# Kernel optimization log

Hardware: AMD Instinct MI355X
Metric: run time of the kernel (lower is better)

Reference implementation:

```python
import jax, jax.numpy as jnp
import numpy as np

N_EMBD = 2048
HEAD_DIM = 128
N_CTX = 2048
BATCH = 8
SEQ = 2048


def setup_inputs() -> dict:
    key = jax.random.key(0)
    ks = jax.random.split(key, 7)
    s = 1.0 / np.sqrt(N_EMBD)
    x = jax.random.normal(ks[0], (BATCH, SEQ, N_EMBD), dtype=jnp.float32)
    # torch Linear params: weight (out, in), bias (out,)
    Wq = jax.random.uniform(ks[1], (HEAD_DIM, N_EMBD), jnp.float32, -s, s)
    bq = jax.random.uniform(ks[2], (HEAD_DIM,), jnp.float32, -s, s)
    Wk = jax.random.uniform(ks[3], (HEAD_DIM, N_EMBD), jnp.float32, -s, s)
    bk = jax.random.uniform(ks[4], (HEAD_DIM,), jnp.float32, -s, s)
    Wv = jax.random.uniform(ks[5], (HEAD_DIM, N_EMBD), jnp.float32, -s, s)
    bv = jax.random.uniform(ks[6], (HEAD_DIM,), jnp.float32, -s, s)
    return {"x": x, "Wq": Wq, "bq": bq, "Wk": Wk, "bk": bk, "Wv": Wv, "bv": bv}


def reference(x, Wq, bq, Wk, bk, Wv, bv):
    # projections: y = x @ W^T + b
    q = jnp.einsum('bse,de->bsd', x, Wq) + bq  # (B, S, D)
    k = jnp.einsum('bse,de->bsd', x, Wk) + bk
    v = jnp.einsum('bse,de->bsd', x, Wv) + bv
    seq = x.shape[1]
    scores = jnp.einsum('bqd,bkd->bqk', q, k)  # (B, S, S)
    # causal mask: strictly-upper-triangular positions set to -inf (before scaling, as in source)
    causal = jnp.triu(jnp.ones((seq, seq), dtype=bool), k=1)
    scores = jnp.where(causal[None, :, :], -jnp.inf, scores)
    # NOTE: source scales by sqrt(seq_size), not sqrt(head_dim)
    weight = jax.nn.softmax(scores / jnp.sqrt(jnp.float32(seq)), axis=-1)
    return jnp.einsum('bqk,bkd->bqd', weight, v)
```

## Files before the change

### kernel.cpp

```cpp
#include <hip/hip_runtime.h>
#include <cmath>

#define BATCH 8
#define SEQ   2048
#define NEMB  2048
#define HD    128
#define NROWS (BATCH * SEQ)

typedef __bf16 v8bf __attribute__((ext_vector_type(8)));
typedef float  f32x4 __attribute__((ext_vector_type(4)));

union U8 { v8bf v; __bf16 b[8]; unsigned short e[8]; };
union F4 { f32x4 v; float f[4]; };

__device__ inline void async16(void* lds, const void* g) {
  __builtin_amdgcn_global_load_lds(
      (const __attribute__((address_space(1))) unsigned int*)g,
      (__attribute__((address_space(3))) unsigned int*)lds, 16, 0, 0);
}

__device__ inline v8bf cvt8(float4 a, float4 b) {
  U8 u;
  u.b[0] = (__bf16)a.x; u.b[1] = (__bf16)a.y; u.b[2] = (__bf16)a.z; u.b[3] = (__bf16)a.w;
  u.b[4] = (__bf16)b.x; u.b[5] = (__bf16)b.y; u.b[6] = (__bf16)b.z; u.b[7] = (__bf16)b.w;
  return u.v;
}

__global__ __launch_bounds__(256) void wconv_kernel(
    const float* __restrict__ Wq, const float* __restrict__ Wk,
    const float* __restrict__ Wv, __bf16* __restrict__ out) {
  const int id = blockIdx.x;
  const int proj = id >> 6, blk = id & 63;
  const float* __restrict__ W = proj == 0 ? Wq : proj == 1 ? Wk : Wv;
  __bf16* __restrict__ o = out + (size_t)proj * (HD * NEMB);
  const int base = blk * 4096 + threadIdx.x * 16;
  const float4* s = (const float4*)(W + base);
  float4 f0 = s[0], f1 = s[1], f2 = s[2], f3 = s[3];
  *(v8bf*)(o + base) = cvt8(f0, f1);
  *(v8bf*)(o + base + 8) = cvt8(f2, f3);
}

__global__ __launch_bounds__(256, 3) void qkv_proj_kernel(
    const float* __restrict__ x, const __bf16* __restrict__ Wb,
    const float* __restrict__ bq, const float* __restrict__ bk,
    const float* __restrict__ bv,
    __bf16* __restrict__ Qb, __bf16* __restrict__ Kb, __bf16* __restrict__ Vb)
{
  const int bid0 = blockIdx.x;
  const int bid = ((bid0 & 7) * 48) + (bid0 >> 3);
  const int mt = bid / 3;
  const int proj = bid % 3;
  const __bf16* __restrict__ W = Wb + (size_t)proj * (HD * NEMB);
  const float* __restrict__ bias = proj == 0 ? bq : proj == 1 ? bk : bv;
  __bf16* __restrict__ Out = proj == 0 ? Qb : proj == 1 ? Kb : Vb;
  const int m0 = mt * 128;

  __shared__ float  Asm[128 * 64];
  __shared__ __bf16 Bsm[128 * 64];

  const int t = threadIdx.x, lane = t & 63, w = t >> 6;
  const int wm = w >> 1, wn = w & 1;
  const int hi = lane >> 4, lo = lane & 15;

  const float* pa[8];
  char* la[8];
#pragma unroll
  for (int i = 0; i < 8; ++i) {
    const int j = w * 8 + i;
    const int r = j * 4 + (lane >> 4);
    const int c = (lane & 15) ^ (r & 7);
    pa[i] = x + (size_t)(m0 + r) * NEMB + c * 4;
    la[i] = (char*)Asm + j * 1024;
  }
  const __bf16* pb[4];
  char* lb[4];
#pragma unroll
  for (int i = 0; i < 4; ++i) {
    const int j = w * 4 + i;
    const int r = j * 8 + (lane >> 3);
    const int c = (lane & 7) ^ (r & 7);
    pb[i] = W + (size_t)r * NEMB + c * 8;
    lb[i] = (char*)Bsm + j * 1024;
  }

  f32x4 acc[4][4];
  const f32x4 fz = {0.f, 0.f, 0.f, 0.f};
#pragma unroll
  for (int m = 0; m < 4; ++m)
#pragma unroll
    for (int n = 0; n < 4; ++n) acc[m][n] = fz;

  for (int tt = 0; tt < NEMB / 64; ++tt) {
    const int k0 = tt * 64;
    __syncthreads();
#pragma unroll
    for (int i = 0; i < 8; ++i) async16(la[i], pa[i] + k0);
#pragma unroll
    for (int i = 0; i < 4; ++i) async16(lb[i], pb[i] + k0);
    __syncthreads();

#pragma unroll
    for (int kk = 0; kk < 2; ++kk) {
      v8bf a[4], b[4];
#pragma unroll
      for (int m = 0; m < 4; ++m) {
        const int r = wm * 64 + m * 16 + lo;
        const int s = kk * 8 + hi * 2;
        const char* rowp = (const char*)Asm + r * 256;
        F4 a0, a1;
        a0.v = *(const f32x4*)(rowp + (((s)     ^ (r & 7)) << 4));
        a1.v = *(const f32x4*)(rowp + (((s + 1) ^ (r & 7)) << 4));
        U8 u;
#pragma unroll
        for (int q = 0; q < 4; ++q) {
          u.b[q]     = (__bf16)a0.f[q];
          u.b[q + 4] = (__bf16)a1.f[q];
        }
        a[m] = u.v;
      }
#pragma unroll
      for (int n = 0; n < 4; ++n) {
        const int r = wn * 64 + n * 16 + lo;
        const int kc = kk * 4 + hi;
        b[n] = *(const v8bf*)((const char*)Bsm + r * 128 + ((kc ^ (r & 7)) << 4));
      }
#pragma unroll
      for (int m = 0; m < 4; ++m)
#pragma unroll
        for (int n = 0; n < 4; ++n)
          acc[m][n] = __builtin_amdgcn_mfma_f32_16x16x32_bf16(a[m], b[n], acc[m][n], 0, 0, 0);
    }
  }

#pragma unroll
  for (int n = 0; n < 4; ++n) {
    const int col = wn * 64 + n * 16 + lo;
    const float bi = bias[col];
#pragma unroll
    for (int m = 0; m < 4; ++m) {
#pragma unroll
      for (int r = 0; r < 4; ++r) {
        const int row = m0 + wm * 64 + m * 16 + hi * 4 + r;
        Out[(size_t)row * HD + col] = (__bf16)(acc[m][n][r] + bi);
      }
    }
  }
}

__global__ __launch_bounds__(256) void attn_kernel(
    const __bf16* __restrict__ Qb, const __bf16* __restrict__ Kb,
    const __bf16* __restrict__ Vb, __bf16* __restrict__ Opart,
    float* __restrict__ Ml)
{
  const int bid0 = blockIdx.x;
  const int bid = ((bid0 & 7) << 7) + (bid0 >> 3);
  const int b = bid >> 7;
  const int q = bid & 127;
  const int qt = q >> 2;
  const int s  = q & 3;
  const int q0 = qt * 64;
  const int kv_beg = (s * (qt + 1)) >> 2;
  const int kv_end = ((s + 1) * (qt + 1)) >> 2;
  const int nst = kv_end - kv_beg;

  const int t = threadIdx.x, lane = t & 63, w = t >> 6;
  const int hi = lane >> 4, lo = lane & 15;

  __shared__ __bf16 Ksm[2][64 * 128];
  __shared__ __bf16 Vtsm[2][128 * 64];
  __shared__ __bf16 Psm[4][16 * 64];

  v8bf aQ[4];
  {
    const __bf16* qp = Qb + ((size_t)(b * SEQ + q0 + w * 16 + lo)) * HD + hi * 8;
#pragma unroll
    for (int kk = 0; kk < 4; ++kk) aQ[kk] = *(const v8bf*)(qp + kk * 32);
  }

  const __bf16* kga[4];
#pragma unroll
  for (int i = 0; i < 4; ++i) {
    const int r = (w * 4 + i) * 4 + (lane >> 4);
    const int c = (lane & 15) ^ (r & 7);
    kga[i] = Kb + ((size_t)(b * SEQ) + r) * HD + c * 8;
  }

  const int keyg = t >> 4, dg = t & 15;
  U8 vv[4];

  f32x4 accO[8];
  const f32x4 fz = {0.f, 0.f, 0.f, 0.f};
#pragma unroll
  for (int n = 0; n < 8; ++n) accO[n] = fz;
  float m_s[4], l_s[4];
#pragma unroll
  for (int r = 0; r < 4; ++r) { m_s[r] = -INFINITY; l_s[r] = 0.f; }

  const float scale = 0.022097086912079608f;

  if (nst > 0) {
    auto STAGE_K = [&](int kv, int buf) {
      const size_t off = (size_t)kv * 64 * HD;
      char* kb = (char*)&Ksm[buf][0];
#pragma unroll
      for (int i = 0; i < 4; ++i) async16(kb + (w * 4 + i) * 1024, kga[i] + off);
    };
    auto LOAD_V = [&](int kv) {
      const __bf16* vp = Vb + ((size_t)(b * SEQ + kv * 64 + keyg * 4)) * HD + dg * 8;
#pragma unroll
      for (int j = 0; j < 4; ++j) vv[j].v = *(const v8bf*)(vp + (size_t)j * HD);
    };
    auto WRITE_VT = [&](int buf) {
      char* vb2 = (char*)&Vtsm[buf][0];
#pragma unroll
      for (int dd = 0; dd < 8; ++dd) {
        const int d = (dd + dg) & 7;
        ushort4 pk = make_ushort4(vv[0].e[d], vv[1].e[d], vv[2].e[d], vv[3].e[d]);
        const int row = dg * 8 + d;
        *(ushort4*)(vb2 + row * 128 + ((keyg * 8) ^ ((row & 7) << 4))) = pk;
      }
    };

    STAGE_K(kv_beg, 0);
    LOAD_V(kv_beg);
    WRITE_VT(0);
    __syncthreads();

    for (int t2 = 0; t2 < nst; ++t2) {
      const int kv = kv_beg + t2;
      const int cur = t2 & 1;
      const bool more = (t2 + 1 < nst);
      if (more) { STAGE_K(kv + 1, cur ^ 1); LOAD_V(kv + 1); }

      f32x4 accS[4];
#pragma unroll
      for (int n = 0; n < 4; ++n) accS[n] = fz;
      const char* ksm = (const char*)&Ksm[cur][0];
#pragma unroll
      for (int kk = 0; kk < 4; ++kk) {
        const int cb = kk * 64 + hi * 16;
        v8bf bk[4];
#pragma unroll
        for (int n = 0; n < 4; ++n) {
          const int r = n * 16 + lo;
          bk[n] = *(const v8bf*)(ksm + r * 256 + (cb ^ ((r & 7) << 4)));
        }
#pragma unroll
        for (int n = 0; n < 4; ++n)
          accS[n] = __builtin_amdgcn_mfma_f32_16x16x32_bf16(aQ[kk], bk[n], accS[n], 0, 0, 0);
      }

      float sv[4][4];
      const bool diag = (kv == qt);
#pragma unroll
      for (int n = 0; n < 4; ++n)
#pragma unroll
        for (int r = 0; r < 4; ++r) {
          float v = accS[n][r] * scale;
          if (diag) {
            const int key = kv * 64 + n * 16 + lo;
            const int qr = q0 + w * 16 + hi * 4 + r;
            if (key > qr) v = -INFINITY;
          }
          sv[n][r] = v;
        }

      float mx[4];
#pragma unroll
      for (int r = 0; r < 4; ++r) {
        mx[r] = fmaxf(fmaxf(sv[0][r], sv[1][r]), fmaxf(sv[2][r], sv[3][r]));
#pragma unroll
        for (int off = 1; off < 16; off <<= 1)
          mx[r] = fmaxf(mx[r], __shfl_xor(mx[r], off));
      }
      float corr[4], p[4][4], rs[4];
#pragma unroll
      for (int r = 0; r < 4; ++r) {
        const float mnew = fmaxf(m_s[r], mx[r]);
        corr[r] = __expf(m_s[r] - mnew);
        m_s[r] = mnew;
        rs[r] = 0.f;
      }
#pragma unroll
      for (int n = 0; n < 4; ++n)
#pragma unroll
        for (int r = 0; r < 4; ++r) {
          p[n][r] = __expf(sv[n][r] - m_s[r]);
          rs[r] += p[n][r];
        }
#pragma unroll
      for (int r = 0; r < 4; ++r) {
#pragma unroll
        for (int off = 1; off < 16; off <<= 1) rs[r] += __shfl_xor(rs[r], off);
        l_s[r] = l_s[r] * corr[r] + rs[r];
      }
#pragma unroll
      for (int n = 0; n < 8; ++n)
#pragma unroll
        for (int r = 0; r < 4; ++r) accO[n][r] *= corr[r];

#pragma unroll
      for (int n = 0; n < 4; ++n)
#pragma unroll
        for (int r = 0; r < 4; ++r) {
          const int row = hi * 4 + r;
          __bf16 h = (__bf16)p[n][r];
          *(unsigned short*)((char*)&Psm[w][0] + row * 128 +
                             (((n * 16 + lo) * 2) ^ ((row & 7) << 4))) =
              __builtin_bit_cast(unsigned short, h);
        }

      if (more) WRITE_VT(cur ^ 1);

      const char* vsm = (const char*)&Vtsm[cur][0];
#pragma unroll
      for (int k2 = 0; k2 < 2; ++k2) {
        const int cb = k2 * 64 + hi * 16;
        const v8bf aP = *(const v8bf*)((const char*)&Psm[w][0] + lo * 128 + (cb ^ ((lo & 7) << 4)));
#pragma unroll
        for (int n = 0; n < 8; ++n) {
          const int r = n * 16 + lo;
          const v8bf bv = *(const v8bf*)(vsm + r * 128 + (cb ^ ((r & 7) << 4)));
          accO[n] = __builtin_amdgcn_mfma_f32_16x16x32_bf16(aP, bv, accO[n], 0, 0, 0);
        }
      }
      if (more) __syncthreads();
    }
  }

#pragma unroll
  for (int r = 0; r < 4; ++r) {
    const int qr = q0 + w * 16 + hi * 4 + r;
    __bf16* op = Opart + ((size_t)s * NROWS + b * SEQ + qr) * HD + lo;
#pragma unroll
    for (int n = 0; n < 8; ++n) op[n * 16] = (__bf16)accO[n][r];
    if (lo == 0) {
      float* mlp = Ml + ((size_t)s * NROWS + b * SEQ + qr) * 2;
      mlp[0] = m_s[r];
      mlp[1] = l_s[r];
    }
  }
}

__global__ __launch_bounds__(256) void combine_kernel(
    const __bf16* __restrict__ Opart, const float* __restrict__ Ml,
    float* __restrict__ out)
{
  const int idx = blockIdx.x * 256 + threadIdx.x;
  const int row = idx >> 2, ch = idx & 3;
  float m[4], l[4];
#pragma unroll
  for (int s = 0; s < 4; ++s) {
    const float* mlp = Ml + ((size_t)s * NROWS + row) * 2;
    m[s] = mlp[0];
    l[s] = mlp[1];
  }
  const float M = fmaxf(fmaxf(m[0], m[1]), fmaxf(m[2], m[3]));
  float e[4], denom = 0.f;
#pragma unroll
  for (int s = 0; s < 4; ++s) { e[s] = __expf(m[s] - M); denom += l[s] * e[s]; }
  const float inv = 1.f / denom;

  float* po = out + (size_t)row * HD + ch * 32;
#pragma unroll
  for (int j = 0; j < 4; ++j) {
    float sum[8];
#pragma unroll
    for (int q2 = 0; q2 < 8; ++q2) sum[q2] = 0.f;
#pragma unroll
    for (int s = 0; s < 4; ++s) {
      U8 o;
      o.v = *(const v8bf*)(Opart + ((size_t)s * NROWS + row) * HD + ch * 32 + j * 8);
#pragma unroll
      for (int q2 = 0; q2 < 8; ++q2) sum[q2] += (float)o.b[q2] * e[s];
    }
#pragma unroll
    for (int q2 = 0; q2 < 8; ++q2) po[j * 8 + q2] = sum[q2] * inv;
  }
}

extern "C" void kernel_launch(void* const* d_in, const int* in_sizes, int n_in,
                              void* d_out, int out_size, void* d_ws, size_t ws_size,
                              hipStream_t stream) {
  const float* x  = (const float*)d_in[0];
  const float* Wq = (const float*)d_in[1];
  const float* bq = (const float*)d_in[2];
  const float* Wk = (const float*)d_in[3];
  const float* bk = (const float*)d_in[4];
  const float* Wv = (const float*)d_in[5];
  const float* bv = (const float*)d_in[6];
  float* out = (float*)d_out;

  __bf16* Qb = (__bf16*)d_ws;
  __bf16* Kb = Qb + (size_t)NROWS * HD;
  __bf16* Vb = Kb + (size_t)NROWS * HD;
  __bf16* Wb = Vb + (size_t)NROWS * HD;
  __bf16* Opart = Wb + (size_t)3 * HD * NEMB;
  float*  Ml = (float*)(Opart + (size_t)4 * NROWS * HD);

  wconv_kernel<<<dim3(3 * 64), dim3(256), 0, stream>>>(Wq, Wk, Wv, Wb);
  qkv_proj_kernel<<<dim3(128 * 3), dim3(256), 0, stream>>>(
      x, Wb, bq, bk, bv, Qb, Kb, Vb);
  attn_kernel<<<dim3(BATCH * 32 * 4), dim3(256), 0, stream>>>(Qb, Kb, Vb, Opart, Ml);
  combine_kernel<<<dim3(NROWS * 4 / 256), dim3(256), 0, stream>>>(Opart, Ml, out);
}
```

Measured before the change: 116.8 us.

## Triple-buffer QKV projection LDS tiles with async prefetch two stages ahead

Converts the QKV projection GEMM main loop from a single-buffered load-sync-compute pattern to a three-stage LDS ring buffer. Tiles for k-step tt+2 are issued via async global-to-LDS loads while step tt computes, with vmcnt waits gating consumption. The aim is to hide global memory latency behind MFMA work. The cost is 144KB of LDS per block, which forces occupancy down to one block per CU, so latency hiding relies entirely on the pipeline.

After: 136.0 us. +16.5%, slower.

```diff
diff --git a/kernel.cpp b/kernel.cpp
--- a/kernel.cpp
+++ b/kernel.cpp
@@ -40,7 +40,7 @@
   *(v8bf*)(o + base + 8) = cvt8(f2, f3);
 }
 
-__global__ __launch_bounds__(256, 3) void qkv_proj_kernel(
+__global__ __launch_bounds__(256, 1) void qkv_proj_kernel(
     const float* __restrict__ x, const __bf16* __restrict__ Wb,
     const float* __restrict__ bq, const float* __restrict__ bk,
     const float* __restrict__ bv,
@@ -55,32 +55,31 @@
   __bf16* __restrict__ Out = proj == 0 ? Qb : proj == 1 ? Kb : Vb;
   const int m0 = mt * 128;
 
-  __shared__ float  Asm[128 * 64];
-  __shared__ __bf16 Bsm[128 * 64];
+  __shared__ char smem[147456];
 
   const int t = threadIdx.x, lane = t & 63, w = t >> 6;
   const int wm = w >> 1, wn = w & 1;
   const int hi = lane >> 4, lo = lane & 15;
 
   const float* pa[8];
-  char* la[8];
+  int laOff[8];
 #pragma unroll
   for (int i = 0; i < 8; ++i) {
     const int j = w * 8 + i;
     const int r = j * 4 + (lane >> 4);
     const int c = (lane & 15) ^ (r & 7);
     pa[i] = x + (size_t)(m0 + r) * NEMB + c * 4;
-    la[i] = (char*)Asm + j * 1024;
+    laOff[i] = j * 1024;
   }
   const __bf16* pb[4];
-  char* lb[4];
+  int lbOff[4];
 #pragma unroll
   for (int i = 0; i < 4; ++i) {
     const int j = w * 4 + i;
     const int r = j * 8 + (lane >> 3);
     const int c = (lane & 7) ^ (r & 7);
     pb[i] = W + (size_t)r * NEMB + c * 8;
-    lb[i] = (char*)Bsm + j * 1024;
+    lbOff[i] = 32768 + j * 1024;
   }
 
   f32x4 acc[4][4];
@@ -90,15 +89,17 @@
 #pragma unroll
     for (int n = 0; n < 4; ++n) acc[m][n] = fz;
 
-  for (int tt = 0; tt < NEMB / 64; ++tt) {
+  auto STAGE = [&](int tt, int buf) {
     const int k0 = tt * 64;
-    __syncthreads();
-#pragma unroll
-    for (int i = 0; i < 8; ++i) async16(la[i], pa[i] + k0);
-#pragma unroll
-    for (int i = 0; i < 4; ++i) async16(lb[i], pb[i] + k0);
-    __syncthreads();
-
+    char* base = smem + buf * 49152;
+#pragma unroll
+    for (int i = 0; i < 8; ++i) async16(base + laOff[i], pa[i] + k0);
+#pragma unroll
+    for (int i = 0; i < 4; ++i) async16(base + lbOff[i], pb[i] + k0);
+  };
+  auto COMPUTE = [&](int buf) {
+    const char* Ab = smem + buf * 49152;
+    const char* Bb = Ab + 32768;
 #pragma unroll
     for (int kk = 0; kk < 2; ++kk) {
       v8bf a[4], b[4];
@@ -106,7 +107,7 @@
       for (int m = 0; m < 4; ++m) {
         const int r = wm * 64 + m * 16 + lo;
         const int s = kk * 8 + hi * 2;
-        const char* rowp = (const char*)Asm + r * 256;
+        const char* rowp = Ab + r * 256;
         F4 a0, a1;
         a0.v = *(const f32x4*)(rowp + (((s)     ^ (r & 7)) << 4));
         a1.v = *(const f32x4*)(rowp + (((s + 1) ^ (r & 7)) << 4));
@@ -122,7 +123,7 @@
       for (int n = 0; n < 4; ++n) {
         const int r = wn * 64 + n * 16 + lo;
         const int kc = kk * 4 + hi;
-        b[n] = *(const v8bf*)((const char*)Bsm + r * 128 + ((kc ^ (r & 7)) << 4));
+        b[n] = *(const v8bf*)(Bb + r * 128 + ((kc ^ (r & 7)) << 4));
       }
 #pragma unroll
       for (int m = 0; m < 4; ++m)
@@ -130,6 +131,22 @@
         for (int n = 0; n < 4; ++n)
           acc[m][n] = __builtin_amdgcn_mfma_f32_16x16x32_bf16(a[m], b[n], acc[m][n], 0, 0, 0);
     }
+  };
+
+  const int NT = NEMB / 64;
+  STAGE(0, 0);
+  STAGE(1, 1);
+  for (int tt = 0; tt < NT; ++tt) {
+    if (tt < NT - 1) {
+      asm volatile("s_waitcnt vmcnt(12)" ::: "memory");
+    } else {
+      asm volatile("s_waitcnt vmcnt(0)" ::: "memory");
+    }
+    __builtin_amdgcn_sched_barrier(0);
+    __builtin_amdgcn_s_barrier();
+    COMPUTE(tt % 3);
+    __builtin_amdgcn_s_barrier();
+    if (tt + 2 < NT) STAGE(tt + 2, (tt + 2) % 3);
   }
 
 #pragma unroll
```

## Split-K the QKV projection with smaller M tiles and a bias-adding reduce kernel

Applied to the files above, without the earlier changes.

The projection GEMM now halves the row tile to 64 and splits the 2048-wide reduction into two halves, raising the grid from 384 to 1536 blocks and the occupancy hint from 3 to 5. The goal is to fill the CUs better than 1.5 waves of large blocks did. Each half writes a bf16 partial result to a new workspace area. A separate reduce kernel then sums the two partials and adds the bias to produce Q, K and V. The cost is an extra launch, extra global traffic for the partials, and an additional bf16 rounding step before the sum.

Measured after the change: 121.2 us. 3.8% more time.

```diff
diff --git a/kernel.cpp b/kernel.cpp
--- a/kernel.cpp
+++ b/kernel.cpp
@@ -40,71 +40,69 @@
   *(v8bf*)(o + base + 8) = cvt8(f2, f3);
 }
 
-__global__ __launch_bounds__(256, 3) void qkv_proj_kernel(
+__global__ __launch_bounds__(256, 5) void qkv_proj_kernel(
     const float* __restrict__ x, const __bf16* __restrict__ Wb,
-    const float* __restrict__ bq, const float* __restrict__ bk,
-    const float* __restrict__ bv,
-    __bf16* __restrict__ Qb, __bf16* __restrict__ Kb, __bf16* __restrict__ Vb)
+    __bf16* __restrict__ Opp)
 {
   const int bid0 = blockIdx.x;
-  const int bid = ((bid0 & 7) * 48) + (bid0 >> 3);
-  const int mt = bid / 3;
-  const int proj = bid % 3;
+  const int bid = ((bid0 & 7) * 192) + (bid0 >> 3);
+  const int mt = bid / 6;
+  const int rem = bid % 6;
+  const int proj = rem >> 1;
+  const int kh = rem & 1;
   const __bf16* __restrict__ W = Wb + (size_t)proj * (HD * NEMB);
-  const float* __restrict__ bias = proj == 0 ? bq : proj == 1 ? bk : bv;
-  __bf16* __restrict__ Out = proj == 0 ? Qb : proj == 1 ? Kb : Vb;
-  const int m0 = mt * 128;
-
-  __shared__ float  Asm[128 * 64];
+  const int m0 = mt * 64;
+  const int kbase = kh * 1024;
+
+  __shared__ float  Asm[64 * 64];
   __shared__ __bf16 Bsm[128 * 64];
 
   const int t = threadIdx.x, lane = t & 63, w = t >> 6;
   const int wm = w >> 1, wn = w & 1;
   const int hi = lane >> 4, lo = lane & 15;
 
-  const float* pa[8];
-  char* la[8];
-#pragma unroll
-  for (int i = 0; i < 8; ++i) {
-    const int j = w * 8 + i;
-    const int r = j * 4 + (lane >> 4);
-    const int c = (lane & 15) ^ (r & 7);
-    pa[i] = x + (size_t)(m0 + r) * NEMB + c * 4;
-    la[i] = (char*)Asm + j * 1024;
-  }
+  const float* pa[4];
   const __bf16* pb[4];
+  char* la[4];
   char* lb[4];
 #pragma unroll
   for (int i = 0; i < 4; ++i) {
-    const int j = w * 4 + i;
-    const int r = j * 8 + (lane >> 3);
-    const int c = (lane & 7) ^ (r & 7);
-    pb[i] = W + (size_t)r * NEMB + c * 8;
-    lb[i] = (char*)Bsm + j * 1024;
-  }
-
-  f32x4 acc[4][4];
+    {
+      const int r = (w * 4 + i) * 4 + (lane >> 4);
+      const int c = (lane & 15) ^ (r & 7);
+      pa[i] = x + (size_t)(m0 + r) * NEMB + kbase + c * 4;
+      la[i] = (char*)Asm + (w * 4 + i) * 1024;
+    }
+    {
+      const int r = (w * 4 + i) * 8 + (lane >> 3);
+      const int c = (lane & 7) ^ (r & 7);
+      pb[i] = W + (size_t)r * NEMB + kbase + c * 8;
+      lb[i] = (char*)Bsm + (w * 4 + i) * 1024;
+    }
+  }
+
+  f32x4 acc[2][4];
   const f32x4 fz = {0.f, 0.f, 0.f, 0.f};
 #pragma unroll
-  for (int m = 0; m < 4; ++m)
+  for (int m = 0; m < 2; ++m)
 #pragma unroll
     for (int n = 0; n < 4; ++n) acc[m][n] = fz;
 
-  for (int tt = 0; tt < NEMB / 64; ++tt) {
+  for (int tt = 0; tt < 16; ++tt) {
     const int k0 = tt * 64;
     __syncthreads();
 #pragma unroll
-    for (int i = 0; i < 8; ++i) async16(la[i], pa[i] + k0);
+    for (int i = 0; i < 4; ++i) async16(la[i], pa[i] + k0);
 #pragma unroll
     for (int i = 0; i < 4; ++i) async16(lb[i], pb[i] + k0);
     __syncthreads();
 
 #pragma unroll
     for (int kk = 0; kk < 2; ++kk) {
-      v8bf a[4], b[4];
-#pragma unroll
-      for (int m = 0; m < 4; ++m) {
-        const int r = wm * 64 + m * 16 + lo;
+      v8bf a[2], b[4];
+#pragma unroll
+      for (int m = 0; m < 2; ++m) {
+        const int r = wm * 32 + m * 16 + lo;
         const int s = kk * 8 + hi * 2;
         const char* rowp = (const char*)Asm + r * 256;
         F4 a0, a1;
@@ -125,26 +123,46 @@
         b[n] = *(const v8bf*)((const char*)Bsm + r * 128 + ((kc ^ (r & 7)) << 4));
       }
 #pragma unroll
-      for (int m = 0; m < 4; ++m)
+      for (int m = 0; m < 2; ++m)
 #pragma unroll
         for (int n = 0; n < 4; ++n)
           acc[m][n] = __builtin_amdgcn_mfma_f32_16x16x32_bf16(a[m], b[n], acc[m][n], 0, 0, 0);
     }
   }
 
+  __bf16* op = Opp + ((size_t)(kh * 3 + proj) * NROWS + m0) * HD;
 #pragma unroll
   for (int n = 0; n < 4; ++n) {
     const int col = wn * 64 + n * 16 + lo;
-    const float bi = bias[col];
-#pragma unroll
-    for (int m = 0; m < 4; ++m) {
+#pragma unroll
+    for (int m = 0; m < 2; ++m) {
 #pragma unroll
       for (int r = 0; r < 4; ++r) {
-        const int row = m0 + wm * 64 + m * 16 + hi * 4 + r;
-        Out[(size_t)row * HD + col] = (__bf16)(acc[m][n][r] + bi);
-      }
-    }
-  }
+        const int row = wm * 32 + m * 16 + hi * 4 + r;
+        op[(size_t)row * HD + col] = (__bf16)acc[m][n][r];
+      }
+    }
+  }
+}
+
+__global__ __launch_bounds__(256) void reduce_kernel(
+    const __bf16* __restrict__ Opp, const float* __restrict__ bq,
+    const float* __restrict__ bk, const float* __restrict__ bv,
+    __bf16* __restrict__ QKV)
+{
+  const size_t g = (size_t)blockIdx.x * 256 + threadIdx.x;
+  const size_t f = g * 8;
+  const int proj = (int)(f / ((size_t)NROWS * HD));
+  const int col = (int)(f & (HD - 1));
+  const float* __restrict__ bias = proj == 0 ? bq : proj == 1 ? bk : bv;
+  U8 p0, p1;
+  p0.v = *(const v8bf*)(Opp + f);
+  p1.v = *(const v8bf*)(Opp + (size_t)3 * NROWS * HD + f);
+  U8 o;
+#pragma unroll
+  for (int j = 0; j < 8; ++j)
+    o.b[j] = (__bf16)((float)p0.b[j] + (float)p1.b[j] + bias[col + j]);
+  *(v8bf*)(QKV + f) = o.v;
 }
 
 __global__ __launch_bounds__(256) void attn_kernel(
@@ -395,12 +413,14 @@
   __bf16* Kb = Qb + (size_t)NROWS * HD;
   __bf16* Vb = Kb + (size_t)NROWS * HD;
   __bf16* Wb = Vb + (size_t)NROWS * HD;
-  __bf16* Opart = Wb + (size_t)3 * HD * NEMB;
+  __bf16* Opp = Wb + (size_t)3 * HD * NEMB;
+  __bf16* Opart = Opp + (size_t)6 * NROWS * HD;
   float*  Ml = (float*)(Opart + (size_t)4 * NROWS * HD);
 
   wconv_kernel<<<dim3(3 * 64), dim3(256), 0, stream>>>(Wq, Wk, Wv, Wb);
-  qkv_proj_kernel<<<dim3(128 * 3), dim3(256), 0, stream>>>(
-      x, Wb, bq, bk, bv, Qb, Kb, Vb);
+  qkv_proj_kernel<<<dim3(1536), dim3(256), 0, stream>>>(x, Wb, Opp);
+  reduce_kernel<<<dim3(3 * NROWS * HD / (256 * 8)), dim3(256), 0, stream>>>(
+      Opp, bq, bk, bv, Qb);
   attn_kernel<<<dim3(BATCH * 32 * 4), dim3(256), 0, stream>>>(Qb, Kb, Vb, Opart, Ml);
   combine_kernel<<<dim3(NROWS * 4 / 256), dim3(256), 0, stream>>>(Opart, Ml, out);
 }
```

## Fuse QKV projections per tile with split-K and fp16 partial reduction

Applied to the files above, without the earlier changes.

The projection kernel now computes Q, K and V together in one 128x384 tile per block, so each x tile is loaded once instead of three times. K is split in half across blocks, giving 256 blocks of 512 threads. Each block writes fp16 partial sums, and a new reduce kernel adds the two halves plus the bias and writes the bf16 Q/K/V. This trades repeated fp32 x traffic for an extra kernel launch, partial-sum memory traffic and a larger workspace, with some risk to fp16 range and precision.

Result: slower. 127.0 us (+8.7%).

```diff
diff --git a/kernel.cpp b/kernel.cpp
--- a/kernel.cpp
+++ b/kernel.cpp
@@ -9,6 +9,7 @@
 
 typedef __bf16 v8bf __attribute__((ext_vector_type(8)));
 typedef float  f32x4 __attribute__((ext_vector_type(4)));
+typedef _Float16 v8h __attribute__((ext_vector_type(8)));
 
 union U8 { v8bf v; __bf16 b[8]; unsigned short e[8]; };
 union F4 { f32x4 v; float f[4]; };
@@ -40,73 +41,71 @@
   *(v8bf*)(o + base + 8) = cvt8(f2, f3);
 }
 
-__global__ __launch_bounds__(256, 3) void qkv_proj_kernel(
+__global__ __launch_bounds__(512, 2) void qkv_proj_kernel(
     const float* __restrict__ x, const __bf16* __restrict__ Wb,
-    const float* __restrict__ bq, const float* __restrict__ bk,
-    const float* __restrict__ bv,
-    __bf16* __restrict__ Qb, __bf16* __restrict__ Kb, __bf16* __restrict__ Vb)
+    _Float16* __restrict__ Opp)
 {
   const int bid0 = blockIdx.x;
-  const int bid = ((bid0 & 7) * 48) + (bid0 >> 3);
-  const int mt = bid / 3;
-  const int proj = bid % 3;
-  const __bf16* __restrict__ W = Wb + (size_t)proj * (HD * NEMB);
-  const float* __restrict__ bias = proj == 0 ? bq : proj == 1 ? bk : bv;
-  __bf16* __restrict__ Out = proj == 0 ? Qb : proj == 1 ? Kb : Vb;
+  const int bid = ((bid0 & 7) << 5) + (bid0 >> 3);
+  const int mt = bid >> 1;
+  const int kh = bid & 1;
   const int m0 = mt * 128;
-
-  __shared__ float  Asm[128 * 64];
-  __shared__ __bf16 Bsm[128 * 64];
+  const int kbase = kh * 1024;
+
+  __shared__ char smem[81920];
+  char* const Asm = smem;
+  char* const Bsm = smem + 32768;
 
   const int t = threadIdx.x, lane = t & 63, w = t >> 6;
-  const int wm = w >> 1, wn = w & 1;
+  const int wm = w >> 2, wn4 = w & 3;
   const int hi = lane >> 4, lo = lane & 15;
 
-  const float* pa[8];
-  char* la[8];
-#pragma unroll
-  for (int i = 0; i < 8; ++i) {
-    const int j = w * 8 + i;
+  const float* pa[4];
+  int laOff[4];
+#pragma unroll
+  for (int i = 0; i < 4; ++i) {
+    const int j = w * 4 + i;
     const int r = j * 4 + (lane >> 4);
     const int c = (lane & 15) ^ (r & 7);
-    pa[i] = x + (size_t)(m0 + r) * NEMB + c * 4;
-    la[i] = (char*)Asm + j * 1024;
-  }
-  const __bf16* pb[4];
-  char* lb[4];
-#pragma unroll
-  for (int i = 0; i < 4; ++i) {
-    const int j = w * 4 + i;
+    pa[i] = x + (size_t)(m0 + r) * NEMB + kbase + c * 4;
+    laOff[i] = j * 1024;
+  }
+  const __bf16* pb[6];
+  int lbOff[6];
+#pragma unroll
+  for (int i = 0; i < 6; ++i) {
+    const int j = w * 6 + i;
     const int r = j * 8 + (lane >> 3);
+    const int pj = r >> 7, wr = r & 127;
     const int c = (lane & 7) ^ (r & 7);
-    pb[i] = W + (size_t)r * NEMB + c * 8;
-    lb[i] = (char*)Bsm + j * 1024;
-  }
-
-  f32x4 acc[4][4];
+    pb[i] = Wb + (size_t)pj * (HD * NEMB) + (size_t)wr * NEMB + kbase + c * 8;
+    lbOff[i] = j * 1024;
+  }
+
+  f32x4 acc[4][6];
   const f32x4 fz = {0.f, 0.f, 0.f, 0.f};
 #pragma unroll
   for (int m = 0; m < 4; ++m)
 #pragma unroll
-    for (int n = 0; n < 4; ++n) acc[m][n] = fz;
-
-  for (int tt = 0; tt < NEMB / 64; ++tt) {
+    for (int n = 0; n < 6; ++n) acc[m][n] = fz;
+
+  for (int tt = 0; tt < 16; ++tt) {
     const int k0 = tt * 64;
     __syncthreads();
 #pragma unroll
-    for (int i = 0; i < 8; ++i) async16(la[i], pa[i] + k0);
-#pragma unroll
-    for (int i = 0; i < 4; ++i) async16(lb[i], pb[i] + k0);
+    for (int i = 0; i < 4; ++i) async16(Asm + laOff[i], pa[i] + k0);
+#pragma unroll
+    for (int i = 0; i < 6; ++i) async16(Bsm + lbOff[i], pb[i] + k0);
     __syncthreads();
 
 #pragma unroll
     for (int kk = 0; kk < 2; ++kk) {
-      v8bf a[4], b[4];
+      v8bf a[4], b[6];
 #pragma unroll
       for (int m = 0; m < 4; ++m) {
         const int r = wm * 64 + m * 16 + lo;
         const int s = kk * 8 + hi * 2;
-        const char* rowp = (const char*)Asm + r * 256;
+        const char* rowp = Asm + r * 256;
         F4 a0, a1;
         a0.v = *(const f32x4*)(rowp + (((s)     ^ (r & 7)) << 4));
         a1.v = *(const f32x4*)(rowp + (((s + 1) ^ (r & 7)) << 4));
@@ -118,33 +117,55 @@
         }
         a[m] = u.v;
       }
-#pragma unroll
-      for (int n = 0; n < 4; ++n) {
-        const int r = wn * 64 + n * 16 + lo;
-        const int kc = kk * 4 + hi;
-        b[n] = *(const v8bf*)((const char*)Bsm + r * 128 + ((kc ^ (r & 7)) << 4));
+      const int kc = kk * 4 + hi;
+#pragma unroll
+      for (int n = 0; n < 6; ++n) {
+        const int r = wn4 * 96 + n * 16 + lo;
+        b[n] = *(const v8bf*)(Bsm + r * 128 + ((kc ^ (r & 7)) << 4));
       }
 #pragma unroll
       for (int m = 0; m < 4; ++m)
 #pragma unroll
-        for (int n = 0; n < 4; ++n)
+        for (int n = 0; n < 6; ++n)
           acc[m][n] = __builtin_amdgcn_mfma_f32_16x16x32_bf16(a[m], b[n], acc[m][n], 0, 0, 0);
     }
   }
 
 #pragma unroll
-  for (int n = 0; n < 4; ++n) {
-    const int col = wn * 64 + n * 16 + lo;
-    const float bi = bias[col];
+  for (int n = 0; n < 6; ++n) {
+    const int rrb = wn4 * 96 + n * 16;
+    const int pj = rrb >> 7;
+    const int col = (rrb & 127) + lo;
+    _Float16* op = Opp + (size_t)(kh * 3 + pj) * NROWS * HD;
 #pragma unroll
     for (int m = 0; m < 4; ++m) {
 #pragma unroll
       for (int r = 0; r < 4; ++r) {
         const int row = m0 + wm * 64 + m * 16 + hi * 4 + r;
-        Out[(size_t)row * HD + col] = (__bf16)(acc[m][n][r] + bi);
+        op[(size_t)row * HD + col] = (_Float16)acc[m][n][r];
       }
     }
   }
+}
+
+__global__ __launch_bounds__(256) void reduce_kernel(
+    const _Float16* __restrict__ Opp, const float* __restrict__ bq,
+    const float* __restrict__ bk, const float* __restrict__ bv,
+    __bf16* __restrict__ QKV)
+{
+  const size_t g = (size_t)blockIdx.x * 256 + threadIdx.x;
+  const size_t f = g * 8;
+  const size_t per = (size_t)NROWS * HD;
+  const int proj = (int)(f / per);
+  const int col = (int)(f & (HD - 1));
+  const float* __restrict__ bias = proj == 0 ? bq : proj == 1 ? bk : bv;
+  v8h p0 = *(const v8h*)(Opp + f);
+  v8h p1 = *(const v8h*)(Opp + (size_t)3 * per + f);
+  U8 o;
+#pragma unroll
+  for (int j = 0; j < 8; ++j)
+    o.b[j] = (__bf16)((float)p0[j] + (float)p1[j] + bias[col + j]);
+  *(v8bf*)(QKV + f) = o.v;
 }
 
 __global__ __launch_bounds__(256) void attn_kernel(
@@ -395,12 +416,14 @@
   __bf16* Kb = Qb + (size_t)NROWS * HD;
   __bf16* Vb = Kb + (size_t)NROWS * HD;
   __bf16* Wb = Vb + (size_t)NROWS * HD;
-  __bf16* Opart = Wb + (size_t)3 * HD * NEMB;
+  _Float16* Opp = (_Float16*)(Wb + (size_t)3 * HD * NEMB);
+  __bf16* Opart = (__bf16*)(Opp + (size_t)6 * NROWS * HD);
   float*  Ml = (float*)(Opart + (size_t)4 * NROWS * HD);
 
   wconv_kernel<<<dim3(3 * 64), dim3(256), 0, stream>>>(Wq, Wk, Wv, Wb);
-  qkv_proj_kernel<<<dim3(128 * 3), dim3(256), 0, stream>>>(
-      x, Wb, bq, bk, bv, Qb, Kb, Vb);
+  qkv_proj_kernel<<<dim3(256), dim3(512), 0, stream>>>(x, Wb, Opp);
+  reduce_kernel<<<dim3(3 * NROWS * HD / (256 * 8)), dim3(256), 0, stream>>>(
+      Opp, bq, bk, bv, Qb);
   attn_kernel<<<dim3(BATCH * 32 * 4), dim3(256), 0, stream>>>(Qb, Kb, Vb, Opart, Ml);
   combine_kernel<<<dim3(NROWS * 4 / 256), dim3(256), 0, stream>>>(Opart, Ml, out);
 }
```
